# Performance work log

Hardware: AMD Instinct MI355X
Metric: run time of the kernel (lower is better)

The kernel has to match this reference:

```python
import jax, jax.numpy as jnp
import numpy as np

B, N, K = 32, 8192, 40


def _pi(x, w, b):
    # permute_invariant_layer: subtract per-(sample,feature) max over set dim,
    # then 1x1 conv1d (pointwise matmul over feature dim).
    x = x - jnp.max(x, axis=2, keepdims=True)          # [B, F, N]
    return jnp.einsum('bfn,of->bon', x, w) + b[None, :, None]


def setup_inputs() -> dict:
    key = jax.random.key(0)
    ks = jax.random.split(key, 12)
    def glorot(k, shape, fan_in):
        return jax.random.normal(k, shape, jnp.float32) * (1.0 / np.sqrt(fan_in))
    return {
        'x': jax.random.normal(ks[0], (B, 3, N), jnp.float32),
        'w1': glorot(ks[1], (64, 3), 3),   'b1': jnp.zeros((64,), jnp.float32),
        'w2': glorot(ks[2], (128, 64), 64), 'b2': jnp.zeros((128,), jnp.float32),
        'w3': glorot(ks[3], (256, 128), 128), 'b3': jnp.zeros((256,), jnp.float32),
        'fc1_w': glorot(ks[4], (128, 256), 256), 'fc1_b': jnp.zeros((128,), jnp.float32),
        'fc2_w': glorot(ks[5], (K, 128), 128),   'fc2_b': jnp.zeros((K,), jnp.float32),
    }


def reference(x, w1, b1, w2, b2, w3, b3, fc1_w, fc1_b, fc2_w, fc2_b):
    h = jnp.tanh(_pi(x, w1, b1))          # [B, 64, N]
    h = jnp.tanh(_pi(h, w2, b2))          # [B, 128, N]
    h = jnp.tanh(_pi(h, w3, b3))          # [B, 256, N]
    g = jnp.max(h, axis=2)                # global max pool -> [B, 256]
    # dropout omitted (deterministic/eval reference)
    g = jnp.tanh(g @ fc1_w.T + fc1_b)     # [B, 128]
    g = jnp.tanh(g @ fc2_w.T + fc2_b)     # [B, K]
    return jax.nn.log_softmax(g, axis=-1)
```

## Files before the change

### kernel.cpp

```cpp
#include <hip/hip_runtime.h>
#include <hip/hip_bf16.h>

#define B_  32
#define N_  8192
#define C1  64
#define C2  128
#define C3  256
#define KO  40
#define SLOTS 8

typedef __attribute__((ext_vector_type(8))) short bh8;
typedef __attribute__((ext_vector_type(4))) float f32x4;

union FragU { uint u[4]; bh8 h; uint4 v; };

#define MFMA_BF16 __builtin_amdgcn_mfma_f32_16x16x32_bf16


__device__ __forceinline__ float ftanh(float x) {
    float e = __expf(2.0f * x);
    float r = __builtin_amdgcn_rcpf(e + 1.0f);
    return fmaf(-2.0f, r, 1.0f);
}

__device__ __forceinline__ float quadMax(float v) {
    v = fmaxf(v, __shfl_xor(v, 1, 64));
    v = fmaxf(v, __shfl_xor(v, 2, 64));
    v = fmaxf(v, __shfl_xor(v, 4, 64));
    v = fmaxf(v, __shfl_xor(v, 8, 64));
    return v;
}

__device__ __forceinline__ unsigned encf(float f) {
    unsigned u = __float_as_uint(f);
    return (u & 0x80000000u) ? ~u : (u | 0x80000000u);
}
__device__ __forceinline__ float decf(unsigned e) {
    return __uint_as_float((e & 0x80000000u) ? (e & 0x7fffffffu) : ~e);
}

__device__ __forceinline__ unsigned packbf(float a, float b) {
    __hip_bfloat162 p = __float22bfloat162_rn(make_float2(a, b));
    unsigned u;
    __builtin_memcpy(&u, &p, 4);
    return u;
}


__global__ __launch_bounds__(128) void k_scan(const float* __restrict__ x,
                                              const float* __restrict__ w1,
                                              const float* __restrict__ w2,
                                              const float* __restrict__ w3,
                                              float* __restrict__ mx1p,
                                              float* __restrict__ mx2p,
                                              uint4* __restrict__ w2f,
                                              uint4* __restrict__ w3f,
                                              unsigned* __restrict__ zeroBase) {
    int t = threadIdx.x;
    int bid = blockIdx.x;
    if (bid < 256) {
        int b = bid >> 3, s = bid & 7;
        const float* xb = x + (size_t)b * 3 * N_ + s * 1024 + t;
        float x0[8], x1[8], x2[8];
#pragma unroll
        for (int i = 0; i < 8; ++i) {
            x0[i] = xb[i * 128];
            x1[i] = xb[N_ + i * 128];
            x2[i] = xb[2 * N_ + i * 128];
        }
        float c0 = x0[0], c1 = x1[0], c2 = x2[0];
#pragma unroll
        for (int i = 1; i < 8; ++i) {
            c0 = fmaxf(c0, x0[i]);
            c1 = fmaxf(c1, x1[i]);
            c2 = fmaxf(c2, x2[i]);
        }
        __shared__ float tl[67][132];
#pragma unroll
        for (int o = 0; o < C1; ++o) {
            float w0 = w1[o * 3 + 0], wa = w1[o * 3 + 1], wb = w1[o * 3 + 2];
            float m = -1e30f;
#pragma unroll
            for (int i = 0; i < 8; ++i)
                m = fmaxf(m, fmaf(x0[i], w0, fmaf(x1[i], wa, x2[i] * wb)));
            tl[o][t] = m;
        }
        tl[64][t] = c0;
        tl[65][t] = c1;
        tl[66][t] = c2;
        __syncthreads();
        if (t < 67) {
            const float4* row = (const float4*)&tl[t][0];
            float4 a0 = row[0], a1 = row[1], a2 = row[2], a3 = row[3];
#pragma unroll
            for (int j = 4; j < 32; j += 4) {
                float4 r0 = row[j], r1 = row[j + 1], r2 = row[j + 2], r3 = row[j + 3];
                a0.x = fmaxf(a0.x, r0.x); a0.y = fmaxf(a0.y, r0.y);
                a0.z = fmaxf(a0.z, r0.z); a0.w = fmaxf(a0.w, r0.w);
                a1.x = fmaxf(a1.x, r1.x); a1.y = fmaxf(a1.y, r1.y);
                a1.z = fmaxf(a1.z, r1.z); a1.w = fmaxf(a1.w, r1.w);
                a2.x = fmaxf(a2.x, r2.x); a2.y = fmaxf(a2.y, r2.y);
                a2.z = fmaxf(a2.z, r2.z); a2.w = fmaxf(a2.w, r2.w);
                a3.x = fmaxf(a3.x, r3.x); a3.y = fmaxf(a3.y, r3.y);
                a3.z = fmaxf(a3.z, r3.z); a3.w = fmaxf(a3.w, r3.w);
            }
            float m = fmaxf(fmaxf(fmaxf(a0.x, a0.y), fmaxf(a0.z, a0.w)),
                            fmaxf(fmaxf(a1.x, a1.y), fmaxf(a1.z, a1.w)));
            m = fmaxf(m, fmaxf(fmaxf(a2.x, a2.y), fmaxf(a2.z, a2.w)));
            m = fmaxf(m, fmaxf(fmaxf(a3.x, a3.y), fmaxf(a3.z, a3.w)));
            if (t < 64) mx2p[(s * 32 + b) * 64 + t] = m;
            else        mx1p[(s * 32 + b) * 4 + (t - 64)] = m;
        }
    } else if (bid < 296) {
        int tid = (bid - 256) * 128 + t;
        const float* src;
        uint4* dst;
        if (tid < 1024) {
            int lane = tid & 63, ks = (tid >> 6) & 1, mt = tid >> 7;
            src = w2 + (mt * 16 + (lane & 15)) * C1 + ks * 32 + (lane >> 4) * 8;
            dst = w2f + tid;
        } else {
            int fj = tid - 1024;
            int lane = fj & 63, ks = (fj >> 6) & 3, mt = fj >> 8;
            src = w3 + (mt * 16 + (lane & 15)) * C2 + ks * 32 + (lane >> 4) * 8;
            dst = w3f + fj;
        }
        uint4 o;
        o.x = packbf(src[0], src[1]);
        o.y = packbf(src[2], src[3]);
        o.z = packbf(src[4], src[5]);
        o.w = packbf(src[6], src[7]);
        *dst = o;
    } else {
        int idx = (bid - 296) * 128 + t;
        for (int i = idx; i < 8192 + 4096; i += 256) zeroBase[i] = 0u;
    }
}


__global__ __launch_bounds__(512) void k_passD(const float* __restrict__ x,
                                               const float* __restrict__ w1,
                                               const float* __restrict__ b1,
                                               const float* __restrict__ w2,
                                               const float* __restrict__ b2,
                                               const float* __restrict__ mx1p,
                                               const float* __restrict__ mx2p,
                                               const uint4* __restrict__ w2f,
                                               const uint4* __restrict__ w3f,
                                               unsigned* __restrict__ mx3e,
                                               unsigned* __restrict__ genc) {
    __shared__ uint4 h1v[8][130];
    __shared__ uint4 h2x[16][130];
    __shared__ float w1s[192];
    __shared__ float beff1s[C1];
    __shared__ float m2s[C1];
    __shared__ float beff2s[C2];

    int b = blockIdx.x >> 6;
    int chunk = blockIdx.x & 63;
    int t = threadIdx.x;
    int p = t & 127, hh = t >> 7;
    int lane = t & 63, wv = t >> 6, qd = lane >> 4, ln = lane & 15;

    const float* xb = x + (size_t)b * 3 * N_ + chunk * 128 + p;
    float x0 = xb[0], x1 = xb[N_], x2 = xb[2 * N_];

    if (t < 192) w1s[t] = w1[t];
    if (t < C1) {
        float mraw = -1e30f;
#pragma unroll
        for (int s = 0; s < SLOTS; ++s)
            mraw = fmaxf(mraw, mx2p[(s * 32 + b) * 64 + t]);
        float s0 = -1e30f, s1 = -1e30f, s2 = -1e30f;
#pragma unroll
        for (int s = 0; s < SLOTS; ++s) {
            s0 = fmaxf(s0, mx1p[(s * 32 + b) * 4 + 0]);
            s1 = fmaxf(s1, mx1p[(s * 32 + b) * 4 + 1]);
            s2 = fmaxf(s2, mx1p[(s * 32 + b) * 4 + 2]);
        }
        float be = b1[t] - s0 * w1[t * 3 + 0] - s1 * w1[t * 3 + 1]
                         - s2 * w1[t * 3 + 2];
        beff1s[t] = be;
        m2s[t] = ftanh(mraw + be);
    }
    __syncthreads();

    if (t < C2) {
        float a = b2[t];
#pragma unroll 8
        for (int f = 0; f < C1; ++f) a -= m2s[f] * w2[t * C1 + f];
        beff2s[t] = a;
    }

#pragma unroll
    for (int qq = 0; qq < 2; ++qq) {
        int c = hh * 16 + qq * 8;
        float v[8];
#pragma unroll
        for (int s = 0; s < 8; ++s) {
            float a = beff1s[c + s];
            a = fmaf(x0, w1s[(c + s) * 3 + 0], a);
            a = fmaf(x1, w1s[(c + s) * 3 + 1], a);
            a = fmaf(x2, w1s[(c + s) * 3 + 2], a);
            v[s] = ftanh(a);
        }
        uint4 pk;
        pk.x = packbf(v[0], v[1]);
        pk.y = packbf(v[2], v[3]);
        pk.z = packbf(v[4], v[5]);
        pk.w = packbf(v[6], v[7]);
        h1v[hh * 2 + qq][p] = pk;
    }
    __syncthreads();

    {
        bh8 wf2[2];
        f32x4 bb2;
#pragma unroll
        for (int ks = 0; ks < 2; ++ks) {
            FragU fu;
            fu.v = w2f[(wv * 2 + ks) * 64 + lane];
            wf2[ks] = fu.h;
        }
#pragma unroll
        for (int r = 0; r < 4; ++r)
            bb2[r] = beff2s[wv * 16 + qd * 4 + r];

        float vmax2[4];
#pragma unroll
        for (int r = 0; r < 4; ++r) vmax2[r] = -1e30f;

        int k4 = wv * 4 + qd;
        uint2* hrow = reinterpret_cast<uint2*>(&h2x[k4 >> 1][0]) + (k4 & 1);

        for (int nb = 0; nb < 8; ++nb) {
            int n = nb * 16 + ln;
            f32x4 acc = bb2;
#pragma unroll
            for (int ks = 0; ks < 2; ++ks) {
                FragU fb;
                fb.v = h1v[ks * 4 + qd][n];
                acc = MFMA_BF16(wf2[ks], fb.h, acc, 0, 0, 0);
            }
#pragma unroll
            for (int r = 0; r < 4; ++r)
                vmax2[r] = fmaxf(vmax2[r], acc[r]);
            hrow[2 * n] = make_uint2(packbf(ftanh(acc[0]), ftanh(acc[1])),
                                     packbf(ftanh(acc[2]), ftanh(acc[3])));
        }
#pragma unroll
        for (int r = 0; r < 4; ++r) {
            float v = quadMax(vmax2[r]);
            if (ln == 0)
                atomicMax(&mx3e[b * C2 + wv * 16 + qd * 4 + r], encf(v));
        }
    }
    __syncthreads();

    {
        bh8 wf3[2][4];
#pragma unroll
        for (int mi = 0; mi < 2; ++mi)
#pragma unroll
            for (int ks = 0; ks < 4; ++ks) {
                FragU fu;
                fu.v = w3f[((2 * wv + mi) * 4 + ks) * 64 + lane];
                wf3[mi][ks] = fu.h;
            }
        float vmax3[2][4];
#pragma unroll
        for (int mi = 0; mi < 2; ++mi)
#pragma unroll
            for (int r = 0; r < 4; ++r) vmax3[mi][r] = -1e30f;

        for (int nb = 0; nb < 8; ++nb) {
            int n = nb * 16 + ln;
            f32x4 acc[2];
#pragma unroll
            for (int mi = 0; mi < 2; ++mi) acc[mi] = (f32x4){0.f, 0.f, 0.f, 0.f};
#pragma unroll
            for (int ks = 0; ks < 4; ++ks) {
                FragU fb;
                fb.v = h2x[ks * 4 + qd][n];
#pragma unroll
                for (int mi = 0; mi < 2; ++mi)
                    acc[mi] = MFMA_BF16(wf3[mi][ks], fb.h, acc[mi], 0, 0, 0);
            }
#pragma unroll
            for (int mi = 0; mi < 2; ++mi)
#pragma unroll
                for (int r = 0; r < 4; ++r)
                    vmax3[mi][r] = fmaxf(vmax3[mi][r], acc[mi][r]);
        }

#pragma unroll
        for (int mi = 0; mi < 2; ++mi)
#pragma unroll
            for (int r = 0; r < 4; ++r) {
                float v = quadMax(vmax3[mi][r]);
                if (ln == 0)
                    atomicMax(&genc[b * C3 + (2 * wv + mi) * 16 + qd * 4 + r], encf(v));
            }
    }
}


__global__ __launch_bounds__(256) void k_fc(const unsigned* __restrict__ mx3e,
                                            const unsigned* __restrict__ genc,
                                            const float* __restrict__ w3,
                                            const float* __restrict__ b3,
                                            const float* __restrict__ fc1w,
                                            const float* __restrict__ fc1b,
                                            const float* __restrict__ fc2w,
                                            const float* __restrict__ fc2b,
                                            float* __restrict__ out) {
    __shared__ float m3[C2];
    __shared__ float gs[C3];
    __shared__ float hs[C2];
    __shared__ float vs[KO];
    __shared__ float red[2];
    int b = blockIdx.x, t = threadIdx.x;
    if (t < C2) m3[t] = ftanh(decf(mx3e[b * C2 + t]));
    __syncthreads();
    {
        float a = b3[t];
#pragma unroll 8
        for (int f = 0; f < C2; ++f) a -= m3[f] * w3[t * C2 + f];
        gs[t] = ftanh(decf(genc[b * C3 + t]) + a);
    }
    __syncthreads();
    if (t < C2) {
        float a = fc1b[t];
#pragma unroll 8
        for (int i = 0; i < C3; ++i) a = fmaf(gs[i], fc1w[t * C3 + i], a);
        hs[t] = ftanh(a);
    }
    __syncthreads();
    if (t < KO) {
        float a = fc2b[t];
#pragma unroll 8
        for (int i = 0; i < C2; ++i) a = fmaf(hs[i], fc2w[t * C2 + i], a);
        vs[t] = ftanh(a);
    }
    __syncthreads();
    if (t == 0) {
        float m = -1e30f;
        for (int j = 0; j < KO; ++j) m = fmaxf(m, vs[j]);
        float s = 0.0f;
        for (int j = 0; j < KO; ++j) s += __expf(vs[j] - m);
        red[0] = m;
        red[1] = __logf(s);
    }
    __syncthreads();
    if (t < KO) out[b * KO + t] = vs[t] - red[0] - red[1];
}


extern "C" void kernel_launch(void* const* d_in, const int* in_sizes, int n_in,
                              void* d_out, int out_size, void* d_ws, size_t ws_size,
                              hipStream_t stream) {
    const float* x    = (const float*)d_in[0];
    const float* w1   = (const float*)d_in[1];
    const float* b1   = (const float*)d_in[2];
    const float* w2   = (const float*)d_in[3];
    const float* b2   = (const float*)d_in[4];
    const float* w3   = (const float*)d_in[5];
    const float* b3   = (const float*)d_in[6];
    const float* fc1w = (const float*)d_in[7];
    const float* fc1b = (const float*)d_in[8];
    const float* fc2w = (const float*)d_in[9];
    const float* fc2b = (const float*)d_in[10];
    float* out = (float*)d_out;

    float* W = (float*)d_ws;
    unsigned* genc = (unsigned*)W;
    unsigned* mx3e = (unsigned*)(W + 8192);
    float*    mx1p = W + 12288;
    float*    mx2p = W + 13312;
    uint4*    w2f  = (uint4*)(W + 29696);
    uint4*    w3f  = (uint4*)(W + 33792);

    k_scan<<<298, 128, 0, stream>>>(x, w1, w2, w3, mx1p, mx2p, w2f, w3f, genc);
    k_passD<<<B_ * 64, 512, 0, stream>>>(x, w1, b1, w2, b2,
                                         mx1p, mx2p, w2f, w3f, mx3e, genc);
    k_fc<<<B_, 256, 0, stream>>>(mx3e, genc, w3, b3, fc1w, fc1b, fc2w, fc2b, out);
}
```

Baseline: 151.6 us.

## Fuse FC head into main pass via last-block counter and relayout h2 LDS

Removes the separate k_fc launch by having the last block per batch (detected via an atomic counter zeroed in k_scan) run the FC head, reading maxima with atomic loads. Also changes the h2 shared buffer to uint2 rows, reading layer-3 fragments as two 8-byte loads. Intends to cut a kernel launch and change LDS bank behavior, at the cost of an extra atomic per block and a tail serialized on 32 blocks.

After: 203.8 us. 1.34x slower.

```diff
diff --git a/kernel.cpp b/kernel.cpp
--- a/kernel.cpp
+++ b/kernel.cpp
@@ -44,6 +44,10 @@
     unsigned u;
     __builtin_memcpy(&u, &p, 4);
     return u;
+}
+
+__device__ __forceinline__ unsigned aload(const unsigned* p) {
+    return __hip_atomic_load(p, __ATOMIC_RELAXED, __HIP_MEMORY_SCOPE_AGENT);
 }
 
 
@@ -133,7 +137,7 @@
         *dst = o;
     } else {
         int idx = (bid - 296) * 128 + t;
-        for (int i = idx; i < 8192 + 4096; i += 256) zeroBase[i] = 0u;
+        for (int i = idx; i < 8192 + 4096 + 64; i += 256) zeroBase[i] = 0u;
     }
 }
 
@@ -143,18 +147,27 @@
                                                const float* __restrict__ b1,
                                                const float* __restrict__ w2,
                                                const float* __restrict__ b2,
+                                               const float* __restrict__ w3,
+                                               const float* __restrict__ b3,
+                                               const float* __restrict__ fc1w,
+                                               const float* __restrict__ fc1b,
+                                               const float* __restrict__ fc2w,
+                                               const float* __restrict__ fc2b,
                                                const float* __restrict__ mx1p,
                                                const float* __restrict__ mx2p,
                                                const uint4* __restrict__ w2f,
                                                const uint4* __restrict__ w3f,
                                                unsigned* __restrict__ mx3e,
-                                               unsigned* __restrict__ genc) {
+                                               unsigned* __restrict__ genc,
+                                               unsigned* __restrict__ cnt,
+                                               float* __restrict__ out) {
     __shared__ uint4 h1v[8][130];
-    __shared__ uint4 h2x[16][130];
+    __shared__ uint2 h2u[32][130];
     __shared__ float w1s[192];
     __shared__ float beff1s[C1];
     __shared__ float m2s[C1];
     __shared__ float beff2s[C2];
+    __shared__ unsigned lastFlag;
 
     int b = blockIdx.x >> 6;
     int chunk = blockIdx.x & 63;
@@ -230,9 +243,6 @@
 #pragma unroll
         for (int r = 0; r < 4; ++r) vmax2[r] = -1e30f;
 
-        int k4 = wv * 4 + qd;
-        uint2* hrow = reinterpret_cast<uint2*>(&h2x[k4 >> 1][0]) + (k4 & 1);
-
         for (int nb = 0; nb < 8; ++nb) {
             int n = nb * 16 + ln;
             f32x4 acc = bb2;
@@ -245,8 +255,8 @@
 #pragma unroll
             for (int r = 0; r < 4; ++r)
                 vmax2[r] = fmaxf(vmax2[r], acc[r]);
-            hrow[2 * n] = make_uint2(packbf(ftanh(acc[0]), ftanh(acc[1])),
-                                     packbf(ftanh(acc[2]), ftanh(acc[3])));
+            h2u[wv * 4 + qd][n] = make_uint2(packbf(ftanh(acc[0]), ftanh(acc[1])),
+                                            packbf(ftanh(acc[2]), ftanh(acc[3])));
         }
 #pragma unroll
         for (int r = 0; r < 4; ++r) {
@@ -280,8 +290,10 @@
             for (int mi = 0; mi < 2; ++mi) acc[mi] = (f32x4){0.f, 0.f, 0.f, 0.f};
 #pragma unroll
             for (int ks = 0; ks < 4; ++ks) {
+                int kk = ks * 4 + qd;
+                uint2 u0 = h2u[2 * kk][n], u1 = h2u[2 * kk + 1][n];
                 FragU fb;
-                fb.v = h2x[ks * 4 + qd][n];
+                fb.u[0] = u0.x; fb.u[1] = u0.y; fb.u[2] = u1.x; fb.u[3] = u1.y;
 #pragma unroll
                 for (int mi = 0; mi < 2; ++mi)
                     acc[mi] = MFMA_BF16(wf3[mi][ks], fb.h, acc[mi], 0, 0, 0);
@@ -302,31 +314,27 @@
                     atomicMax(&genc[b * C3 + (2 * wv + mi) * 16 + qd * 4 + r], encf(v));
             }
     }
-}
-
-
-__global__ __launch_bounds__(256) void k_fc(const unsigned* __restrict__ mx3e,
-                                            const unsigned* __restrict__ genc,
-                                            const float* __restrict__ w3,
-                                            const float* __restrict__ b3,
-                                            const float* __restrict__ fc1w,
-                                            const float* __restrict__ fc1b,
-                                            const float* __restrict__ fc2w,
-                                            const float* __restrict__ fc2b,
-                                            float* __restrict__ out) {
-    __shared__ float m3[C2];
-    __shared__ float gs[C3];
-    __shared__ float hs[C2];
-    __shared__ float vs[KO];
-    __shared__ float red[2];
-    int b = blockIdx.x, t = threadIdx.x;
-    if (t < C2) m3[t] = ftanh(decf(mx3e[b * C2 + t]));
-    __syncthreads();
-    {
+
+    if (t == 0) {
+        unsigned old = __hip_atomic_fetch_add(&cnt[b], 1u, __ATOMIC_ACQ_REL,
+                                              __HIP_MEMORY_SCOPE_AGENT);
+        lastFlag = (old == 63u) ? 1u : 0u;
+    }
+    __syncthreads();
+    if (!lastFlag) return;
+
+    float* m3  = (float*)&h1v[0][0];
+    float* gs  = m3 + C2;
+    float* hs  = gs + C3;
+    float* vs  = hs + C2;
+    float* red = vs + KO;
+    if (t < C2) m3[t] = ftanh(decf(aload(&mx3e[b * C2 + t])));
+    __syncthreads();
+    if (t < C3) {
         float a = b3[t];
 #pragma unroll 8
         for (int f = 0; f < C2; ++f) a -= m3[f] * w3[t * C2 + f];
-        gs[t] = ftanh(decf(genc[b * C3 + t]) + a);
+        gs[t] = ftanh(decf(aload(&genc[b * C3 + t])) + a);
     }
     __syncthreads();
     if (t < C2) {
@@ -375,13 +383,14 @@
     float* W = (float*)d_ws;
     unsigned* genc = (unsigned*)W;
     unsigned* mx3e = (unsigned*)(W + 8192);
-    float*    mx1p = W + 12288;
-    float*    mx2p = W + 13312;
-    uint4*    w2f  = (uint4*)(W + 29696);
-    uint4*    w3f  = (uint4*)(W + 33792);
+    unsigned* cnt  = (unsigned*)(W + 12288);
+    float*    mx1p = W + 12352;
+    float*    mx2p = W + 13376;
+    uint4*    w2f  = (uint4*)(W + 29760);
+    uint4*    w3f  = (uint4*)(W + 33856);
 
     k_scan<<<298, 128, 0, stream>>>(x, w1, w2, w3, mx1p, mx2p, w2f, w3f, genc);
-    k_passD<<<B_ * 64, 512, 0, stream>>>(x, w1, b1, w2, b2,
-                                         mx1p, mx2p, w2f, w3f, mx3e, genc);
-    k_fc<<<B_, 256, 0, stream>>>(mx3e, genc, w3, b3, fc1w, fc1b, fc2w, fc2b, out);
-}
+    k_passD<<<B_ * 64, 512, 0, stream>>>(x, w1, b1, w2, b2, w3, b3,
+                                         fc1w, fc1b, fc2w, fc2b,
+                                         mx1p, mx2p, w2f, w3f, mx3e, genc, cnt, out);
+}
```
